# Kernel optimization log

Measured on AMD Instinct MI355X. Metric: run time of the kernel, lower is better.

The kernel has to match this reference:

```python
import jax, jax.numpy as jnp
import numpy as np

EMBEDDING_DIM = 64
N_EMBEDDINGS = 512


def setup_inputs() -> dict:
    key = jax.random.key(0)
    k1, k2 = jax.random.split(key)
    inputs = jax.random.normal(k1, (32, 64, 64, 64), dtype=jnp.float32)  # NCHW, C==embedding_dim
    weight = jax.random.normal(k2, (N_EMBEDDINGS, EMBEDDING_DIM), dtype=jnp.float32)
    return {"inputs": inputs, "weight": weight}


def reference(inputs, weight):
    # NCHW -> NHWC, flatten to [N, D]
    x = jnp.transpose(inputs, (0, 2, 3, 1))  # [B, H, W, D]
    in_shape = x.shape
    flat = x.reshape(-1, EMBEDDING_DIM)  # [N, D]

    distances = (
        jnp.sum(flat * flat, axis=1, keepdims=True)
        + jnp.sum(weight * weight, axis=1)
        - 2.0 * flat @ weight.T
    )
    idx = jnp.argmin(distances, axis=1)  # [N]

    # one-hot @ weight is just a gather
    quantized = weight[idx].reshape(in_shape)  # [B, H, W, D]

    # commitment loss: mse(stop_grad(quantized), x)
    e_latent_loss = jnp.mean(jnp.square(jax.lax.stop_gradient(quantized) - x))

    # straight-through estimator
    quantized = x + jax.lax.stop_gradient(quantized - x)

    return jnp.transpose(quantized, (0, 3, 1, 2)), e_latent_loss
```

## Files before the change

kernel.cpp:

```cpp
#include <hip/hip_runtime.h>
#include <math.h>

typedef short bf16x8 __attribute__((ext_vector_type(8)));
typedef float f32x4 __attribute__((ext_vector_type(4)));

#define VQ_D 64
#define VQ_K 512
#define VQ_NQ 131072
#define VQ_TOTAL 8388608
#define NT 32
#define NC 16
#define TAU 8e-3f

typedef __attribute__((address_space(1))) void as1_void;
typedef __attribute__((address_space(3))) void as3_void;

__device__ __forceinline__ void gll16(const void* g, void* l) {
    __builtin_amdgcn_global_load_lds((as1_void*)(void*)g, (as3_void*)l, 16, 0, 0);
}
__device__ __forceinline__ void gll4(const void* g, void* l) {
    __builtin_amdgcn_global_load_lds((as1_void*)(void*)g, (as3_void*)l, 4, 0, 0);
}

__device__ __forceinline__ ushort bf16_rne(float f) {
    uint u = __builtin_bit_cast(uint, f);
    u += 0x7fffu + ((u >> 16) & 1u);
    return (ushort)(u >> 16);
}
__device__ __forceinline__ float bf16_to_f(ushort h) {
    uint u = ((uint)h) << 16;
    return __builtin_bit_cast(float, u);
}

__global__ __launch_bounds__(128) void vq_prep(const float* __restrict__ w,
                                               ushort* __restrict__ wfrag,
                                               float* __restrict__ wn,
                                               float* __restrict__ out) {
    if (blockIdx.x == 0 && threadIdx.x == 0) out[VQ_TOTAL] = 0.f;
    const int tid = threadIdx.x;
    const int k = (blockIdx.x << 4) + (tid >> 3);
    const int g = tid & 7;
    const float4* row = (const float4*)(w + k * VQ_D);
    float4 a = row[2 * g], b4 = row[2 * g + 1];
    float v[8] = {a.x, a.y, a.z, a.w, b4.x, b4.y, b4.z, b4.w};
    ushort hi[8], lo[8];
    float nrm = 0.f;
#pragma unroll
    for (int j = 0; j < 8; ++j) {
        nrm = fmaf(v[j], v[j], nrm);
        hi[j] = bf16_rne(v[j]);
        lo[j] = bf16_rne(v[j] - bf16_to_f(hi[j]));
    }
    nrm += __shfl_xor(nrm, 1, 64);
    nrm += __shfl_xor(nrm, 2, 64);
    nrm += __shfl_xor(nrm, 4, 64);
    if (g == 0) wn[k] = nrm;
    const int t = k >> 4, col = k & 15;
    const int quad = g & 3, fh = g >> 2;
    bf16x8* basez = (bf16x8*)wfrag + t * 256 + quad * 16 + col;
    basez[fh * 64]       = *(bf16x8*)hi;
    basez[(2 + fh) * 64] = *(bf16x8*)lo;
}

__global__ __launch_bounds__(256, 4) void vq_main(const float* __restrict__ in,
                                                  const float* __restrict__ w,
                                                  const ushort* __restrict__ wfrag,
                                                  const float* __restrict__ wng,
                                                  float* __restrict__ out) {
    __shared__ __align__(16) char bstage[2][8192];
    __shared__ float wn_lds[VQ_K];
    __shared__ float xn_lds[128];
    __shared__ float best_lds[128], sec_lds[128];
    __shared__ int   bi_lds[128], si_lds[128];

    const int tid  = threadIdx.x;
    const int lane = tid & 63;
    const int wid  = tid >> 6;
    const int col  = lane & 15;
    const int quad = lane >> 4;
    const int n0  = blockIdx.x * 128;
    const int b   = n0 >> 12;
    const int hw0 = n0 & 4095;
    const float* xg0 = in + (b << 18) + hw0;
    const float* xgW = xg0 + wid * 32;

    {
        const char* gs = (const char*)wfrag + tid * 16;
        char* lb = &bstage[0][0] + wid * 1024;
        gll16(gs, lb);
        gll16(gs + 4096, lb + 4096);
        gll4(wng + tid,       (char*)wn_lds + wid * 256);
        gll4(wng + 256 + tid, (char*)wn_lds + 1024 + wid * 256);
    }

    bf16x8 ah0[2], ah1[2], al0[2], al1[2];
#pragma unroll
    for (int T = 0; T < 2; ++T) {
        const float* xq = xgW + T * 16 + col;
        float sx = 0.f;
        ushort h0[8], l0[8], h1[8], l1[8];
#pragma unroll
        for (int j = 0; j < 8; ++j) {
            float v0 = xq[(quad * 8 + j) << 12];
            float v1 = xq[(32 + quad * 8 + j) << 12];
            sx = fmaf(v0, v0, sx);
            sx = fmaf(v1, v1, sx);
            h0[j] = bf16_rne(v0); l0[j] = bf16_rne(v0 - bf16_to_f(h0[j]));
            h1[j] = bf16_rne(v1); l1[j] = bf16_rne(v1 - bf16_to_f(h1[j]));
        }
        ah0[T] = *(bf16x8*)h0; al0[T] = *(bf16x8*)l0;
        ah1[T] = *(bf16x8*)h1; al1[T] = *(bf16x8*)l1;
        sx += __shfl_xor(sx, 16, 64);
        sx += __shfl_xor(sx, 32, 64);
        if (quad == 0) xn_lds[wid * 32 + T * 16 + col] = sx;
    }

    __syncthreads();

    float best[8], sec[8];
#pragma unroll
    for (int r = 0; r < 8; ++r) { best[r] = 3.0e38f; sec[r] = 3.0e38f; }

#pragma unroll 1
    for (int t = 0; t < NC; ++t) {
        char* const bcur = &bstage[t & 1][0];
        if (t + 1 < NC) {
            const char* gs = (const char*)wfrag + (t + 1) * 8192 + tid * 16;
            char* lb = &bstage[(t + 1) & 1][0] + wid * 1024;
            gll16(gs, lb);
            gll16(gs + 4096, lb + 4096);
        }
#pragma unroll
        for (int s = 0; s < 2; ++s) {
            const int t2 = 2 * t + s;
            const char* rb = bcur + s * 4096 + lane * 16;
            bf16x8 bh0 = *(const bf16x8*)(rb);
            bf16x8 bh1 = *(const bf16x8*)(rb + 1024);
            bf16x8 bl0 = *(const bf16x8*)(rb + 2048);
            bf16x8 bl1 = *(const bf16x8*)(rb + 3072);
            const float wnv = wn_lds[t2 * 16 + col];
#pragma unroll
            for (int T = 0; T < 2; ++T) {
                f32x4 accP = {0.f, 0.f, 0.f, 0.f}, accQ = {0.f, 0.f, 0.f, 0.f};
                __builtin_amdgcn_s_setprio(1);
                accP = __builtin_amdgcn_mfma_f32_16x16x32_bf16(ah0[T], bh0, accP, 0, 0, 0);
                accP = __builtin_amdgcn_mfma_f32_16x16x32_bf16(ah1[T], bh1, accP, 0, 0, 0);
                accQ = __builtin_amdgcn_mfma_f32_16x16x32_bf16(ah0[T], bl0, accQ, 0, 0, 0);
                accQ = __builtin_amdgcn_mfma_f32_16x16x32_bf16(ah1[T], bl1, accQ, 0, 0, 0);
                accQ = __builtin_amdgcn_mfma_f32_16x16x32_bf16(al0[T], bh0, accQ, 0, 0, 0);
                accQ = __builtin_amdgcn_mfma_f32_16x16x32_bf16(al1[T], bh1, accQ, 0, 0, 0);
                __builtin_amdgcn_s_setprio(0);
#pragma unroll
                for (int j = 0; j < 4; ++j) {
                    float dist = fmaf(-2.f, accP[j] + accQ[j], wnv);
                    uint u = (__builtin_bit_cast(uint, dist) & 0xFFFFFFE0u) | (uint)t2;
                    float key = __builtin_bit_cast(float, u);
                    const int r = T * 4 + j;
                    float m = fmaxf(best[r], key);
                    best[r] = fminf(best[r], key);
                    sec[r]  = fminf(sec[r], m);
                }
            }
        }
        __syncthreads();
    }

    float bD[8], sD[8];
    int bI[8], sI[8];
#pragma unroll
    for (int r = 0; r < 8; ++r) {
        uint ub = __builtin_bit_cast(uint, best[r]);
        uint us = __builtin_bit_cast(uint, sec[r]);
        bI[r] = (int)(ub & 31u) * 16 + col;
        sI[r] = (int)(us & 31u) * 16 + col;
        bD[r] = __builtin_bit_cast(float, ub & 0xFFFFFFE0u);
        sD[r] = __builtin_bit_cast(float, us & 0xFFFFFFE0u);
    }

#pragma unroll
    for (int off = 1; off < 16; off <<= 1) {
#pragma unroll
        for (int r = 0; r < 8; ++r) {
            float ob = __shfl_xor(bD[r], off, 64);
            float os = __shfl_xor(sD[r], off, 64);
            int   oi = __shfl_xor(bI[r], off, 64);
            int   oc = __shfl_xor(sI[r], off, 64);
            bool oWins = (ob < bD[r]) || (ob == bD[r] && oi < bI[r]);
            float nb  = oWins ? ob    : bD[r];
            int   ni  = oWins ? oi    : bI[r];
            float c1  = oWins ? bD[r] : ob;
            int   ci1 = oWins ? bI[r] : oi;
            float c2  = oWins ? os    : sD[r];
            int   ci2 = oWins ? oc    : sI[r];
            bool c1w = (c1 < c2) || (c1 == c2 && ci1 < ci2);
            sD[r] = c1w ? c1  : c2;
            sI[r] = c1w ? ci1 : ci2;
            bD[r] = nb; bI[r] = ni;
        }
    }
    if (col == 0) {
#pragma unroll
        for (int r = 0; r < 8; ++r) {
            const int q = wid * 32 + (r >> 2) * 16 + quad * 4 + (r & 3);
            best_lds[q] = bD[r]; sec_lds[q] = sD[r];
            bi_lds[q] = bI[r];   si_lds[q] = sI[r];
        }
    }
    __syncthreads();

    if (tid < 128) {
        const int q = tid;
        float cb = best_lds[q], cs = sec_lds[q];
        int cbi = bi_lds[q], csi = si_lds[q];
        double chosen = (double)cb;
        if (cs - cb < TAU) {
            const float* wb  = w + cbi * VQ_D;
            const float* ws2 = w + csi * VQ_D;
            const float* xqp = xg0 + q;
            double nb = 0.0, dotb = 0.0, ns = 0.0, dots = 0.0;
            for (int d = 0; d < VQ_D; ++d) {
                double xv = (double)xqp[d << 12];
                double wbv = (double)wb[d], wsv = (double)ws2[d];
                nb = fma(wbv, wbv, nb); dotb = fma(xv, wbv, dotb);
                ns = fma(wsv, wsv, ns); dots = fma(xv, wsv, dots);
            }
            double db = nb - 2.0 * dotb, ds = ns - 2.0 * dots;
            if (ds < db || (ds == db && csi < cbi)) { cbi = csi; chosen = ds; }
            else                                    { chosen = db; }
        }
        bi_lds[q] = cbi;
        double lq = (double)xn_lds[q] + chosen;
#pragma unroll
        for (int off = 32; off > 0; off >>= 1)
            lq += __shfl_down(lq, off, 64);
        if ((tid & 63) == 0)
            atomicAdd(out + VQ_TOTAL, (float)(lq * (1.0 / (double)VQ_TOTAL)));
    }
    __syncthreads();

    {
        const int q = tid & 127, half = tid >> 7;
        const float4* wrow = (const float4*)(w + bi_lds[q] * VQ_D) + half * 8;
        float* op = out + (b << 18) + hw0 + q;
#pragma unroll
        for (int u = 0; u < 8; ++u) {
            float4 v = wrow[u];
            const int d = half * 32 + 4 * u;
            op[(d + 0) << 12] = v.x;
            op[(d + 1) << 12] = v.y;
            op[(d + 2) << 12] = v.z;
            op[(d + 3) << 12] = v.w;
        }
    }
}

extern "C" void kernel_launch(void* const* d_in, const int* in_sizes, int n_in,
                              void* d_out, int out_size, void* d_ws, size_t ws_size,
                              hipStream_t stream) {
    const float* in = (const float*)d_in[0];
    const float* w  = (const float*)d_in[1];
    float* out = (float*)d_out;

    ushort* wfrag = (ushort*)d_ws;
    float*  wn    = (float*)((char*)d_ws + 131072);

    vq_prep<<<32, 128, 0, stream>>>(w, wfrag, wn, out);
    vq_main<<<VQ_NQ / 128, 256, 0, stream>>>(in, w, wfrag, wn, out);
}
```

Measured before the change: 132.6 us.

## Double block to 512 threads, one 16-query tile per wave, larger codebook chunks

Each block now runs 8 waves, and each wave handles 16 queries instead of 32. This halves the per-thread register state (A fragments, best/second keys) and should allow more waves per CU. The codebook is staged in 16 KB chunks over 8 iterations instead of 8 KB over 16, which halves the number of block barriers. The fp64 tie-break refinement is split across 4 lanes per query with shuffle reduction, and the per-block loss is reduced through LDS to one atomic. The cost is that every B fragment loaded from LDS is reused for only one MFMA tile per wave instead of two, which increases LDS read traffic per MFMA, and the larger blocks make barriers more expensive.

Result: faster. 116.7 us (-12.0%).

```diff
diff --git a/kernel.cpp b/kernel.cpp
--- a/kernel.cpp
+++ b/kernel.cpp
@@ -9,7 +9,7 @@
 #define VQ_NQ 131072
 #define VQ_TOTAL 8388608
 #define NT 32
-#define NC 16
+#define NCK 8
 #define TAU 8e-3f
 
 typedef __attribute__((address_space(1))) void as1_void;
@@ -62,16 +62,17 @@
     basez[(2 + fh) * 64] = *(bf16x8*)lo;
 }
 
-__global__ __launch_bounds__(256, 4) void vq_main(const float* __restrict__ in,
+__global__ __launch_bounds__(512, 8) void vq_main(const float* __restrict__ in,
                                                   const float* __restrict__ w,
                                                   const ushort* __restrict__ wfrag,
                                                   const float* __restrict__ wng,
                                                   float* __restrict__ out) {
-    __shared__ __align__(16) char bstage[2][8192];
+    __shared__ __align__(16) char bstage[2][16384];
     __shared__ float wn_lds[VQ_K];
     __shared__ float xn_lds[128];
     __shared__ float best_lds[128], sec_lds[128];
     __shared__ int   bi_lds[128], si_lds[128];
+    __shared__ double loss_lds[8];
 
     const int tid  = threadIdx.x;
     const int lane = tid & 63;
@@ -82,21 +83,18 @@
     const int b   = n0 >> 12;
     const int hw0 = n0 & 4095;
     const float* xg0 = in + (b << 18) + hw0;
-    const float* xgW = xg0 + wid * 32;
 
     {
         const char* gs = (const char*)wfrag + tid * 16;
         char* lb = &bstage[0][0] + wid * 1024;
         gll16(gs, lb);
-        gll16(gs + 4096, lb + 4096);
-        gll4(wng + tid,       (char*)wn_lds + wid * 256);
-        gll4(wng + 256 + tid, (char*)wn_lds + 1024 + wid * 256);
-    }
-
-    bf16x8 ah0[2], ah1[2], al0[2], al1[2];
-#pragma unroll
-    for (int T = 0; T < 2; ++T) {
-        const float* xq = xgW + T * 16 + col;
+        gll16(gs + 8192, lb + 8192);
+        gll4(wng + tid, (char*)wn_lds + wid * 256);
+    }
+
+    bf16x8 ah0, ah1, al0, al1;
+    {
+        const float* xq = xg0 + wid * 16 + col;
         float sx = 0.f;
         ushort h0[8], l0[8], h1[8], l1[8];
 #pragma unroll
@@ -108,67 +106,63 @@
             h0[j] = bf16_rne(v0); l0[j] = bf16_rne(v0 - bf16_to_f(h0[j]));
             h1[j] = bf16_rne(v1); l1[j] = bf16_rne(v1 - bf16_to_f(h1[j]));
         }
-        ah0[T] = *(bf16x8*)h0; al0[T] = *(bf16x8*)l0;
-        ah1[T] = *(bf16x8*)h1; al1[T] = *(bf16x8*)l1;
+        ah0 = *(bf16x8*)h0; al0 = *(bf16x8*)l0;
+        ah1 = *(bf16x8*)h1; al1 = *(bf16x8*)l1;
         sx += __shfl_xor(sx, 16, 64);
         sx += __shfl_xor(sx, 32, 64);
-        if (quad == 0) xn_lds[wid * 32 + T * 16 + col] = sx;
+        if (quad == 0) xn_lds[wid * 16 + col] = sx;
     }
 
     __syncthreads();
 
-    float best[8], sec[8];
-#pragma unroll
-    for (int r = 0; r < 8; ++r) { best[r] = 3.0e38f; sec[r] = 3.0e38f; }
+    float best[4], sec[4];
+#pragma unroll
+    for (int r = 0; r < 4; ++r) { best[r] = 3.0e38f; sec[r] = 3.0e38f; }
 
 #pragma unroll 1
-    for (int t = 0; t < NC; ++t) {
-        char* const bcur = &bstage[t & 1][0];
-        if (t + 1 < NC) {
-            const char* gs = (const char*)wfrag + (t + 1) * 8192 + tid * 16;
-            char* lb = &bstage[(t + 1) & 1][0] + wid * 1024;
+    for (int c = 0; c < NCK; ++c) {
+        char* const bcur = &bstage[c & 1][0];
+        if (c + 1 < NCK) {
+            const char* gs = (const char*)wfrag + (c + 1) * 16384 + tid * 16;
+            char* lb = &bstage[(c + 1) & 1][0] + wid * 1024;
             gll16(gs, lb);
-            gll16(gs + 4096, lb + 4096);
-        }
-#pragma unroll
-        for (int s = 0; s < 2; ++s) {
-            const int t2 = 2 * t + s;
+            gll16(gs + 8192, lb + 8192);
+        }
+#pragma unroll
+        for (int s = 0; s < 4; ++s) {
+            const int t2 = 4 * c + s;
             const char* rb = bcur + s * 4096 + lane * 16;
             bf16x8 bh0 = *(const bf16x8*)(rb);
             bf16x8 bh1 = *(const bf16x8*)(rb + 1024);
             bf16x8 bl0 = *(const bf16x8*)(rb + 2048);
             bf16x8 bl1 = *(const bf16x8*)(rb + 3072);
             const float wnv = wn_lds[t2 * 16 + col];
-#pragma unroll
-            for (int T = 0; T < 2; ++T) {
-                f32x4 accP = {0.f, 0.f, 0.f, 0.f}, accQ = {0.f, 0.f, 0.f, 0.f};
-                __builtin_amdgcn_s_setprio(1);
-                accP = __builtin_amdgcn_mfma_f32_16x16x32_bf16(ah0[T], bh0, accP, 0, 0, 0);
-                accP = __builtin_amdgcn_mfma_f32_16x16x32_bf16(ah1[T], bh1, accP, 0, 0, 0);
-                accQ = __builtin_amdgcn_mfma_f32_16x16x32_bf16(ah0[T], bl0, accQ, 0, 0, 0);
-                accQ = __builtin_amdgcn_mfma_f32_16x16x32_bf16(ah1[T], bl1, accQ, 0, 0, 0);
-                accQ = __builtin_amdgcn_mfma_f32_16x16x32_bf16(al0[T], bh0, accQ, 0, 0, 0);
-                accQ = __builtin_amdgcn_mfma_f32_16x16x32_bf16(al1[T], bh1, accQ, 0, 0, 0);
-                __builtin_amdgcn_s_setprio(0);
-#pragma unroll
-                for (int j = 0; j < 4; ++j) {
-                    float dist = fmaf(-2.f, accP[j] + accQ[j], wnv);
-                    uint u = (__builtin_bit_cast(uint, dist) & 0xFFFFFFE0u) | (uint)t2;
-                    float key = __builtin_bit_cast(float, u);
-                    const int r = T * 4 + j;
-                    float m = fmaxf(best[r], key);
-                    best[r] = fminf(best[r], key);
-                    sec[r]  = fminf(sec[r], m);
-                }
+            f32x4 accP = {0.f, 0.f, 0.f, 0.f}, accQ = {0.f, 0.f, 0.f, 0.f};
+            __builtin_amdgcn_s_setprio(1);
+            accP = __builtin_amdgcn_mfma_f32_16x16x32_bf16(ah0, bh0, accP, 0, 0, 0);
+            accP = __builtin_amdgcn_mfma_f32_16x16x32_bf16(ah1, bh1, accP, 0, 0, 0);
+            accQ = __builtin_amdgcn_mfma_f32_16x16x32_bf16(ah0, bl0, accQ, 0, 0, 0);
+            accQ = __builtin_amdgcn_mfma_f32_16x16x32_bf16(ah1, bl1, accQ, 0, 0, 0);
+            accQ = __builtin_amdgcn_mfma_f32_16x16x32_bf16(al0, bh0, accQ, 0, 0, 0);
+            accQ = __builtin_amdgcn_mfma_f32_16x16x32_bf16(al1, bh1, accQ, 0, 0, 0);
+            __builtin_amdgcn_s_setprio(0);
+#pragma unroll
+            for (int j = 0; j < 4; ++j) {
+                float dist = fmaf(-2.f, accP[j] + accQ[j], wnv);
+                uint u = (__builtin_bit_cast(uint, dist) & 0xFFFFFFE0u) | (uint)t2;
+                float key = __builtin_bit_cast(float, u);
+                float m = fmaxf(best[j], key);
+                best[j] = fminf(best[j], key);
+                sec[j]  = fminf(sec[j], m);
             }
         }
         __syncthreads();
     }
 
-    float bD[8], sD[8];
-    int bI[8], sI[8];
-#pragma unroll
-    for (int r = 0; r < 8; ++r) {
+    float bD[4], sD[4];
+    int bI[4], sI[4];
+#pragma unroll
+    for (int r = 0; r < 4; ++r) {
         uint ub = __builtin_bit_cast(uint, best[r]);
         uint us = __builtin_bit_cast(uint, sec[r]);
         bI[r] = (int)(ub & 31u) * 16 + col;
@@ -180,7 +174,7 @@
 #pragma unroll
     for (int off = 1; off < 16; off <<= 1) {
 #pragma unroll
-        for (int r = 0; r < 8; ++r) {
+        for (int r = 0; r < 4; ++r) {
             float ob = __shfl_xor(bD[r], off, 64);
             float os = __shfl_xor(sD[r], off, 64);
             int   oi = __shfl_xor(bI[r], off, 64);
@@ -200,52 +194,66 @@
     }
     if (col == 0) {
 #pragma unroll
-        for (int r = 0; r < 8; ++r) {
-            const int q = wid * 32 + (r >> 2) * 16 + quad * 4 + (r & 3);
+        for (int r = 0; r < 4; ++r) {
+            const int q = wid * 16 + quad * 4 + r;
             best_lds[q] = bD[r]; sec_lds[q] = sD[r];
             bi_lds[q] = bI[r];   si_lds[q] = sI[r];
         }
     }
     __syncthreads();
 
-    if (tid < 128) {
-        const int q = tid;
+    {
+        const int q = tid >> 2, part = tid & 3;
         float cb = best_lds[q], cs = sec_lds[q];
         int cbi = bi_lds[q], csi = si_lds[q];
         double chosen = (double)cb;
         if (cs - cb < TAU) {
-            const float* wb  = w + cbi * VQ_D;
-            const float* ws2 = w + csi * VQ_D;
+            const float* wb  = w + cbi * VQ_D + part * 16;
+            const float* ws2 = w + csi * VQ_D + part * 16;
             const float* xqp = xg0 + q;
             double nb = 0.0, dotb = 0.0, ns = 0.0, dots = 0.0;
-            for (int d = 0; d < VQ_D; ++d) {
+#pragma unroll
+            for (int d0 = 0; d0 < 16; ++d0) {
+                const int d = part * 16 + d0;
                 double xv = (double)xqp[d << 12];
-                double wbv = (double)wb[d], wsv = (double)ws2[d];
+                double wbv = (double)wb[d0], wsv = (double)ws2[d0];
                 nb = fma(wbv, wbv, nb); dotb = fma(xv, wbv, dotb);
                 ns = fma(wsv, wsv, ns); dots = fma(xv, wsv, dots);
+            }
+#pragma unroll
+            for (int off = 1; off < 4; off <<= 1) {
+                nb   += __shfl_xor(nb,   off, 64);
+                dotb += __shfl_xor(dotb, off, 64);
+                ns   += __shfl_xor(ns,   off, 64);
+                dots += __shfl_xor(dots, off, 64);
             }
             double db = nb - 2.0 * dotb, ds = ns - 2.0 * dots;
             if (ds < db || (ds == db && csi < cbi)) { cbi = csi; chosen = ds; }
             else                                    { chosen = db; }
         }
-        bi_lds[q] = cbi;
-        double lq = (double)xn_lds[q] + chosen;
+        if (part == 0) bi_lds[q] = cbi;
+        double lq = (part == 0) ? ((double)xn_lds[q] + chosen) : 0.0;
 #pragma unroll
         for (int off = 32; off > 0; off >>= 1)
             lq += __shfl_down(lq, off, 64);
-        if ((tid & 63) == 0)
-            atomicAdd(out + VQ_TOTAL, (float)(lq * (1.0 / (double)VQ_TOTAL)));
+        if (lane == 0) loss_lds[wid] = lq;
     }
     __syncthreads();
-
-    {
-        const int q = tid & 127, half = tid >> 7;
-        const float4* wrow = (const float4*)(w + bi_lds[q] * VQ_D) + half * 8;
+    if (tid == 0) {
+        double s = 0.0;
+#pragma unroll
+        for (int wv = 0; wv < 8; ++wv) s += loss_lds[wv];
+        atomicAdd(out + VQ_TOTAL, (float)(s * (1.0 / (double)VQ_TOTAL)));
+    }
+
+    {
+        const int q = tid & 127, quarter = tid >> 7;
+        const float4* wrow = (const float4*)(w + bi_lds[q] * VQ_D) + quarter * 4;
         float* op = out + (b << 18) + hw0 + q;
 #pragma unroll
-        for (int u = 0; u < 8; ++u) {
+        for (int u = 0; u < 4; ++u) {
             float4 v = wrow[u];
-            const int d = half * 32 + 4 * u;
+            const int d = quarter * 16 + 4 * u;
             op[(d + 0) << 12] = v.x;
             op[(d + 1) << 12] = v.y;
             op[(d + 2) << 12] = v.z;
@@ -265,5 +273,5 @@
     float*  wn    = (float*)((char*)d_ws + 131072);
 
     vq_prep<<<32, 128, 0, stream>>>(w, wfrag, wn, out);
-    vq_main<<<VQ_NQ / 128, 256, 0, stream>>>(in, w, wfrag, wn, out);
-}
+    vq_main<<<VQ_NQ / 128, 512, 0, stream>>>(in, w, wfrag, wn, out);
+}
```
